# Kernel optimization log

Hardware: AMD Instinct MI355X
Metric: run time of the kernel (lower is better)

Reference implementation:

```python
import jax, jax.numpy as jnp
import numpy as np

N, E, G = 50000, 800000, 64
IN, H, C = 128, 3, 64
HC = H * C


def _conv(x, src, dst, Wq, bq, Wk, bk, Wv, bv, Ws, bs, Wb):
    # node-level projections, then per-edge gather
    q = (x @ Wq + bq).reshape(-1, H, C)[dst]   # [E,H,C]
    k = (x @ Wk + bk).reshape(-1, H, C)[src]
    v = (x @ Wv + bv).reshape(-1, H, C)[src]
    alpha = (q * k).sum(-1) / jnp.sqrt(jnp.float32(C))  # [E,H]
    # segment softmax over incoming edges of each target node
    amax = jax.ops.segment_max(alpha, dst, num_segments=N)
    amax = jnp.where(jnp.isfinite(amax), amax, 0.0)
    ex = jnp.exp(alpha - amax[dst])
    denom = jax.ops.segment_sum(ex, dst, num_segments=N)
    a = ex / (denom[dst] + 1e-16)
    out = jax.ops.segment_sum(a[:, :, None] * v, dst, num_segments=N).reshape(-1, HC)
    # gated skip (beta=True, root_weight=True)
    r = x @ Ws + bs
    beta = jax.nn.sigmoid(jnp.concatenate([out, r, out - r], -1) @ Wb)  # [N,1]
    return beta * r + (1.0 - beta) * out


def setup_inputs() -> dict:
    key = jax.random.key(0)
    ks = jax.random.split(key, 32)
    x = jax.random.normal(ks[0], (N, IN), dtype=jnp.float32)
    edge_index = jax.random.randint(ks[1], (2, E), 0, N, dtype=jnp.int32)
    batch = jnp.sort(jax.random.randint(ks[2], (N,), 0, G, dtype=jnp.int32))
    s = 0.05
    def w(k, shape):
        return jax.random.normal(k, shape, dtype=jnp.float32) * s
    d = {"x": x, "edge_index": edge_index, "batch": batch}
    ins = [IN, HC]
    ki = 3
    for l in range(2):
        din = ins[l]
        d[f"Wq{l}"] = w(ks[ki], (din, HC)); ki += 1
        d[f"bq{l}"] = jnp.zeros((HC,), jnp.float32)
        d[f"Wk{l}"] = w(ks[ki], (din, HC)); ki += 1
        d[f"bk{l}"] = jnp.zeros((HC,), jnp.float32)
        d[f"Wv{l}"] = w(ks[ki], (din, HC)); ki += 1
        d[f"bv{l}"] = jnp.zeros((HC,), jnp.float32)
        d[f"Ws{l}"] = w(ks[ki], (din, HC)); ki += 1
        d[f"bs{l}"] = jnp.zeros((HC,), jnp.float32)
        d[f"Wb{l}"] = w(ks[ki], (3 * HC, 1)); ki += 1
    d["Wlin"] = w(ks[ki], (HC, 1)); ki += 1
    d["blin"] = jnp.zeros((1,), jnp.float32)
    return d


def reference(x, edge_index, batch,
              Wq0, bq0, Wk0, bk0, Wv0, bv0, Ws0, bs0, Wb0,
              Wq1, bq1, Wk1, bk1, Wv1, bv1, Ws1, bs1, Wb1,
              Wlin, blin):
    src, dst = edge_index[0], edge_index[1]
    h = _conv(x, src, dst, Wq0, bq0, Wk0, bk0, Wv0, bv0, Ws0, bs0, Wb0)
    h = jax.nn.elu(h)
    h = _conv(h, src, dst, Wq1, bq1, Wk1, bk1, Wv1, bv1, Ws1, bs1, Wb1)
    h = jax.nn.elu(h)
    # global mean pool over graphs
    cnt = jax.ops.segment_sum(jnp.ones((N,), jnp.float32), batch, num_segments=G)
    pooled = jax.ops.segment_sum(h, batch, num_segments=G) / jnp.maximum(cnt, 1.0)[:, None]
    logits = (pooled @ Wlin + blin).squeeze(-1)  # [G]
    return logits
```

## Files before the change

kernel.cpp:

```cpp
#include <hip/hip_runtime.h>
#include <math.h>

#define NNODES 50000
#define NEDGES 800000
#define NGRAPH 64
#define DIM_IN 128
#define HCDIM  192
#define QKVRW  768

typedef __attribute__((ext_vector_type(8))) short short8;
typedef __attribute__((ext_vector_type(4))) float f32x4;
typedef __attribute__((ext_vector_type(2))) float f32x2;

__device__ __forceinline__ unsigned short f2bf(float f){
  unsigned int u = __float_as_uint(f);
  unsigned int r = (u + 0x7fffu + ((u>>16)&1u)) >> 16;
  return (unsigned short)r;
}

__device__ __forceinline__ float4 bf4_to_f4(uint2 u){
  float4 f;
  f.x = __uint_as_float(u.x<<16);
  f.y = __uint_as_float(u.x & 0xffff0000u);
  f.z = __uint_as_float(u.y<<16);
  f.w = __uint_as_float(u.y & 0xffff0000u);
  return f;
}

__device__ __forceinline__ float4 fp8x4_to_f4(unsigned int u){
  f32x2 lo = __builtin_amdgcn_cvt_pk_f32_fp8((int)u, false);
  f32x2 hi = __builtin_amdgcn_cvt_pk_f32_fp8((int)u, true);
  float4 f; f.x=lo[0]; f.y=lo[1]; f.z=hi[0]; f.w=hi[1];
  return f;
}

__device__ __forceinline__ float wave_sum(float v){
#pragma unroll
  for(int off=32; off>0; off>>=1) v += __shfl_xor(v, off, 64);
  return v;
}

__global__ void zero_i(int* p, int n){
  int i = blockIdx.x*blockDim.x + threadIdx.x;
  if(i<n) p[i]=0;
}

__global__ void zero2_k(int* a, int* b, int n){
  int i = blockIdx.x*blockDim.x + threadIdx.x;
  if(i<n){ a[i]=0; b[i]=0; }
}

__global__ void hist_k(const int* __restrict__ dst, int* __restrict__ counts, int E){
  int e = blockIdx.x*blockDim.x + threadIdx.x;
  if(e<E) atomicAdd(&counts[dst[e]], 1);
}

__global__ void scan_partial(const int* __restrict__ counts, int* __restrict__ bsum, int N){
  __shared__ int lds[256];
  int t = threadIdx.x;
  int idx = blockIdx.x*256 + t;
  int v = (idx<N)? counts[idx] : 0;
  lds[t]=v; __syncthreads();
#pragma unroll
  for(int off=128; off>0; off>>=1){
    if(t<off) lds[t]+=lds[t+off];
    __syncthreads();
  }
  if(t==0) bsum[blockIdx.x]=lds[0];
}

__global__ void scan_bsum(int* bsum, int nb){
  __shared__ int lds[1024];
  int t=threadIdx.x;
  int v=(t<nb)?bsum[t]:0;
  lds[t]=v; __syncthreads();
  int x=v;
#pragma unroll
  for(int off=1; off<1024; off<<=1){
    int y=(t>=off)?lds[t-off]:0;
    __syncthreads();
    x+=y; lds[t]=x;
    __syncthreads();
  }
  if(t<nb) bsum[t]=x-v;
}

__global__ void scan_final(const int* __restrict__ counts, const int* __restrict__ bsum,
                           int* __restrict__ row_ptr, int N){
  __shared__ int lds[256];
  int t=threadIdx.x;
  int idx=blockIdx.x*256+t;
  int v=(idx<N)?counts[idx]:0;
  lds[t]=v; __syncthreads();
  int x=v;
#pragma unroll
  for(int off=1; off<256; off<<=1){
    int y=(t>=off)?lds[t-off]:0;
    __syncthreads();
    x+=y; lds[t]=x;
    __syncthreads();
  }
  if(idx<=N) row_ptr[idx]= bsum[blockIdx.x]+x-v;
}

__global__ void fill_k(const int* __restrict__ src, const int* __restrict__ dst,
                       const int* __restrict__ row_ptr, int* __restrict__ cursor,
                       int* __restrict__ csr_src, int E){
  int e = blockIdx.x*blockDim.x + threadIdx.x;
  if(e<E){
    int d = dst[e];
    int pos = row_ptr[d] + atomicAdd(&cursor[d], 1);
    csr_src[pos] = src[e];
  }
}

__global__ void cast_bf16(const float* __restrict__ X, unsigned short* __restrict__ Xb, int n4){
  int i = blockIdx.x*blockDim.x + threadIdx.x;
  int i4 = i*4;
  if(i4 < n4){
    float4 v = *(const float4*)(X+i4);
    ushort4 o; o.x=f2bf(v.x); o.y=f2bf(v.y); o.z=f2bf(v.z); o.w=f2bf(v.w);
    *(ushort4*)(Xb+i4) = o;
  }
}

__global__ void build_wt(const float* __restrict__ Wq, const float* __restrict__ Wk,
                         const float* __restrict__ Wv, const float* __restrict__ Ws,
                         const float* __restrict__ bq, const float* __restrict__ bk,
                         const float* __restrict__ bv, const float* __restrict__ bs,
                         unsigned short* __restrict__ Wt, float* __restrict__ bcat, int K){
  int idx = blockIdx.x*256 + threadIdx.x;
  if(idx < QKVRW*K){
    int c = idx / K, k = idx % K;
    int mat = c/HCDIM, cm = c%HCDIM;
    const float* W = (mat==0)?Wq:(mat==1)?Wk:(mat==2)?Wv:Ws;
    Wt[(size_t)c*K + k] = f2bf(W[(size_t)k*HCDIM + cm]);
  }
  if(idx < QKVRW){
    int mat = idx/HCDIM, cm = idx%HCDIM;
    const float* b = (mat==0)?bq:(mat==1)?bk:(mat==2)?bv:bs;
    bcat[idx] = b[cm];
  }
}

template<int K>
__global__ __launch_bounds__(256) void gemm_mfma(
    const unsigned short* __restrict__ Xb,
    const unsigned short* __restrict__ Wt,
    const float* __restrict__ bcat,
    unsigned short* __restrict__ QR,
    unsigned char* __restrict__ KV, int N)
{
  constexpr int CPR = K/8;
  __shared__ unsigned short As[128*K];
  __shared__ unsigned short Bs[64*K];
  const int tid = threadIdx.x;
  const int wv = tid>>6;
  const int lane = tid&63;
  const int m0  = blockIdx.x*128;
  const int cb  = blockIdx.y;
  const int mat = cb/3;
  const int nc0 = cb*64;

  constexpr int A_IT = 128*CPR/256;
#pragma unroll
  for(int it=0; it<A_IT; ++it){
    int p = it*256 + tid;
    int r = p/CPR, c = p%CPR;
    int cs = c ^ (r&7);
    int grow = m0 + r; if(grow > N-1) grow = N-1;
    const unsigned short* gp = Xb + (size_t)grow*K + cs*8;
    unsigned short* lp = As + (size_t)(it*256 + wv*64)*8;
    __builtin_amdgcn_global_load_lds(
        (const __attribute__((address_space(1))) unsigned int*)gp,
        (__attribute__((address_space(3))) unsigned int*)lp, 16, 0, 0);
  }
  constexpr int B_IT = 64*CPR/256;
#pragma unroll
  for(int it=0; it<B_IT; ++it){
    int p = it*256 + tid;
    int r = p/CPR, c = p%CPR;
    int cs = c ^ (r&7);
    const unsigned short* gp = Wt + (size_t)(nc0 + r)*K + cs*8;
    unsigned short* lp = Bs + (size_t)(it*256 + wv*64)*8;
    __builtin_amdgcn_global_load_lds(
        (const __attribute__((address_space(1))) unsigned int*)gp,
        (__attribute__((address_space(3))) unsigned int*)lp, 16, 0, 0);
  }
  __syncthreads();

  const int wr = wv>>1, wc = wv&1;
  const int lhi = lane>>4, llo = lane&15;
  f32x4 acc[4][2] = {};
#pragma unroll
  for(int kk=0; kk<K; kk+=32){
    short8 a[4], b[2];
    const int chunk = kk/8 + lhi;
#pragma unroll
    for(int i=0;i<4;++i){
      int rr = wr*64 + i*16 + llo;
      int cs = chunk ^ (rr&7);
      a[i] = *(const short8*)(As + (size_t)rr*K + cs*8);
    }
#pragma unroll
    for(int j=0;j<2;++j){
      int cc = wc*32 + j*16 + llo;
      int cs = chunk ^ (cc&7);
      b[j] = *(const short8*)(Bs + (size_t)cc*K + cs*8);
    }
#pragma unroll
    for(int i=0;i<4;++i)
#pragma unroll
      for(int j=0;j<2;++j)
        acc[i][j] = __builtin_amdgcn_mfma_f32_16x16x32_bf16(a[i], b[j], acc[i][j], 0,0,0);
  }

  const int col0 = nc0 + wc*32 + llo;
  float bias0 = bcat[col0];
  float bias1 = bcat[col0+16];
  if(mat==0 || mat==3){
    const int coff = (mat==0) ? col0 : col0-384;
#pragma unroll
    for(int i=0;i<4;++i){
#pragma unroll
      for(int r=0;r<4;++r){
        int grow = m0 + wr*64 + i*16 + lhi*4 + r;
        if(grow < N){
          size_t base = (size_t)grow*384 + coff;
          QR[base]      = f2bf(acc[i][0][r] + bias0);
          QR[base + 16] = f2bf(acc[i][1][r] + bias1);
        }
      }
    }
  } else {
#pragma unroll
    for(int i=0;i<4;++i){
#pragma unroll
      for(int r=0;r<4;++r){
        int grow = m0 + wr*64 + i*16 + lhi*4 + r;
        float v0 = acc[i][0][r] + bias0;
        float v1 = acc[i][1][r] + bias1;
        float n0 = __shfl_xor(v0, 1, 64);
        float n1 = __shfl_xor(v1, 1, 64);
        if(((llo&1)==0) && grow < N){
          int p0 = __builtin_amdgcn_cvt_pk_fp8_f32(v0, n0, 0, false);
          int p1 = __builtin_amdgcn_cvt_pk_fp8_f32(v1, n1, 0, false);
          unsigned char* kb = KV + (size_t)grow*384 + (col0-192);
          *(unsigned short*)(kb)    = (unsigned short)(p0 & 0xffff);
          *(unsigned short*)(kb+16) = (unsigned short)(p1 & 0xffff);
        }
      }
    }
  }
}

template<bool OUTBF>
__global__ __launch_bounds__(256) void attn_kernel(
  const unsigned short* __restrict__ QR,
  const unsigned char* __restrict__ KV,
  const int* __restrict__ row_ptr, const int* __restrict__ csr_src,
  const float* __restrict__ Wb, float* __restrict__ HoutF,
  unsigned short* __restrict__ HoutB, int N)
{
  const int wave = threadIdx.x>>6;
  const int lane = threadIdx.x&63;
  const int g    = lane>>4;
  const int l    = lane&15;
  const int n = blockIdx.x*4 + wave;
  if(n>=N) return;

  const unsigned short* nr = QR + (size_t)n*384 + 4*l;
  float4 q0 = bf4_to_f4(*(const uint2*)(nr));
  float4 q1 = bf4_to_f4(*(const uint2*)(nr+64));
  float4 q2 = bf4_to_f4(*(const uint2*)(nr+128));

  const int s0 = row_ptr[n];
  const int deg = row_ptr[n+1]-s0;

  float4 a0={0,0,0,0}, a1={0,0,0,0}, a2={0,0,0,0};
  float d0=0.f,d1=0.f,d2=0.f;

  int sCur = csr_src[s0 + (g<deg ? g : 0)];
  for(int base=0; base<deg; base+=4){
    const int inext = base + 4 + g;
    const int sNxt = csr_src[s0 + (inext<deg ? inext : 0)];
    const bool valid = (base + g < deg);
    const unsigned int* kv = (const unsigned int*)(KV + (size_t)sCur*384) + l;
    unsigned int ku0 = kv[0],  ku1 = kv[16], ku2 = kv[32];
    unsigned int vu0 = kv[48], vu1 = kv[64], vu2 = kv[80];
    float4 k0 = fp8x4_to_f4(ku0);
    float4 k1 = fp8x4_to_f4(ku1);
    float4 k2 = fp8x4_to_f4(ku2);
    float p0 = q0.x*k0.x+q0.y*k0.y+q0.z*k0.z+q0.w*k0.w;
    float p1 = q1.x*k1.x+q1.y*k1.y+q1.z*k1.z+q1.w*k1.w;
    float p2 = q2.x*k2.x+q2.y*k2.y+q2.z*k2.z+q2.w*k2.w;
#pragma unroll
    for(int off=1; off<16; off<<=1){
      p0 += __shfl_xor(p0, off, 64);
      p1 += __shfl_xor(p1, off, 64);
      p2 += __shfl_xor(p2, off, 64);
    }
    float e0 = valid ? __expf(0.125f*p0) : 0.f;
    float e1 = valid ? __expf(0.125f*p1) : 0.f;
    float e2 = valid ? __expf(0.125f*p2) : 0.f;
    d0 += e0; d1 += e1; d2 += e2;
    float4 v0 = fp8x4_to_f4(vu0);
    float4 v1 = fp8x4_to_f4(vu1);
    float4 v2 = fp8x4_to_f4(vu2);
    a0.x+=e0*v0.x; a0.y+=e0*v0.y; a0.z+=e0*v0.z; a0.w+=e0*v0.w;
    a1.x+=e1*v1.x; a1.y+=e1*v1.y; a1.z+=e1*v1.z; a1.w+=e1*v1.w;
    a2.x+=e2*v2.x; a2.y+=e2*v2.y; a2.z+=e2*v2.z; a2.w+=e2*v2.w;
    sCur = sNxt;
  }

#pragma unroll
  for(int off=16; off<64; off<<=1){
    a0.x+=__shfl_xor(a0.x,off,64); a0.y+=__shfl_xor(a0.y,off,64);
    a0.z+=__shfl_xor(a0.z,off,64); a0.w+=__shfl_xor(a0.w,off,64);
    a1.x+=__shfl_xor(a1.x,off,64); a1.y+=__shfl_xor(a1.y,off,64);
    a1.z+=__shfl_xor(a1.z,off,64); a1.w+=__shfl_xor(a1.w,off,64);
    a2.x+=__shfl_xor(a2.x,off,64); a2.y+=__shfl_xor(a2.y,off,64);
    a2.z+=__shfl_xor(a2.z,off,64); a2.w+=__shfl_xor(a2.w,off,64);
    d0+=__shfl_xor(d0,off,64); d1+=__shfl_xor(d1,off,64); d2+=__shfl_xor(d2,off,64);
  }
  const float id0=1.f/(d0+1e-16f), id1=1.f/(d1+1e-16f), id2=1.f/(d2+1e-16f);
  float4 o0, o1, o2;
  o0.x=a0.x*id0; o0.y=a0.y*id0; o0.z=a0.z*id0; o0.w=a0.w*id0;
  o1.x=a1.x*id1; o1.y=a1.y*id1; o1.z=a1.z*id1; o1.w=a1.w*id1;
  o2.x=a2.x*id2; o2.y=a2.y*id2; o2.z=a2.z*id2; o2.w=a2.w*id2;

  float4 r0 = bf4_to_f4(*(const uint2*)(nr+192));
  float4 r1 = bf4_to_f4(*(const uint2*)(nr+256));
  float4 r2 = bf4_to_f4(*(const uint2*)(nr+320));

  const float* wb = Wb + 4*l;
  float4 w00=*(const float4*)(wb),     w01=*(const float4*)(wb+64),  w02=*(const float4*)(wb+128);
  float4 w10=*(const float4*)(wb+192), w11=*(const float4*)(wb+256), w12=*(const float4*)(wb+320);
  float4 w20=*(const float4*)(wb+384), w21=*(const float4*)(wb+448), w22=*(const float4*)(wb+512);
  float z =
    o0.x*w00.x+o0.y*w00.y+o0.z*w00.z+o0.w*w00.w +
    o1.x*w01.x+o1.y*w01.y+o1.z*w01.z+o1.w*w01.w +
    o2.x*w02.x+o2.y*w02.y+o2.z*w02.z+o2.w*w02.w +
    r0.x*w10.x+r0.y*w10.y+r0.z*w10.z+r0.w*w10.w +
    r1.x*w11.x+r1.y*w11.y+r1.z*w11.z+r1.w*w11.w +
    r2.x*w12.x+r2.y*w12.y+r2.z*w12.z+r2.w*w12.w +
    (o0.x-r0.x)*w20.x+(o0.y-r0.y)*w20.y+(o0.z-r0.z)*w20.z+(o0.w-r0.w)*w20.w +
    (o1.x-r1.x)*w21.x+(o1.y-r1.y)*w21.y+(o1.z-r1.z)*w21.z+(o1.w-r1.w)*w21.w +
    (o2.x-r2.x)*w22.x+(o2.y-r2.y)*w22.y+(o2.z-r2.z)*w22.z+(o2.w-r2.w)*w22.w;
#pragma unroll
  for(int off=1; off<16; off<<=1) z += __shfl_xor(z, off, 64);
  const float beta = 1.f/(1.f+__expf(-z));
  float4 h0,h1,h2;
  h0.x=beta*r0.x+(1.f-beta)*o0.x; h0.y=beta*r0.y+(1.f-beta)*o0.y;
  h0.z=beta*r0.z+(1.f-beta)*o0.z; h0.w=beta*r0.w+(1.f-beta)*o0.w;
  h1.x=beta*r1.x+(1.f-beta)*o1.x; h1.y=beta*r1.y+(1.f-beta)*o1.y;
  h1.z=beta*r1.z+(1.f-beta)*o1.z; h1.w=beta*r1.w+(1.f-beta)*o1.w;
  h2.x=beta*r2.x+(1.f-beta)*o2.x; h2.y=beta*r2.y+(1.f-beta)*o2.y;
  h2.z=beta*r2.z+(1.f-beta)*o2.z; h2.w=beta*r2.w+(1.f-beta)*o2.w;
  h0.x=(h0.x>0.f)?h0.x:expm1f(h0.x); h0.y=(h0.y>0.f)?h0.y:expm1f(h0.y);
  h0.z=(h0.z>0.f)?h0.z:expm1f(h0.z); h0.w=(h0.w>0.f)?h0.w:expm1f(h0.w);
  h1.x=(h1.x>0.f)?h1.x:expm1f(h1.x); h1.y=(h1.y>0.f)?h1.y:expm1f(h1.y);
  h1.z=(h1.z>0.f)?h1.z:expm1f(h1.z); h1.w=(h1.w>0.f)?h1.w:expm1f(h1.w);
  h2.x=(h2.x>0.f)?h2.x:expm1f(h2.x); h2.y=(h2.y>0.f)?h2.y:expm1f(h2.y);
  h2.z=(h2.z>0.f)?h2.z:expm1f(h2.z); h2.w=(h2.w>0.f)?h2.w:expm1f(h2.w);
  if(g==0){
    if(OUTBF){
      unsigned short* hb = HoutB + (size_t)n*HCDIM + 4*l;
      ushort4 u0, u1, u2;
      u0.x=f2bf(h0.x); u0.y=f2bf(h0.y); u0.z=f2bf(h0.z); u0.w=f2bf(h0.w);
      u1.x=f2bf(h1.x); u1.y=f2bf(h1.y); u1.z=f2bf(h1.z); u1.w=f2bf(h1.w);
      u2.x=f2bf(h2.x); u2.y=f2bf(h2.y); u2.z=f2bf(h2.z); u2.w=f2bf(h2.w);
      *(ushort4*)(hb)     = u0;
      *(ushort4*)(hb+64)  = u1;
      *(ushort4*)(hb+128) = u2;
    } else {
      float* ho = HoutF + (size_t)n*HCDIM + 4*l;
      *(float4*)(ho)     = h0;
      *(float4*)(ho+64)  = h1;
      *(float4*)(ho+128) = h2;
    }
  }
}

__global__ void zero_pool(float* pooled, int* cnt){
  int i = blockIdx.x*256 + threadIdx.x;
  if(i < NGRAPH*HCDIM) ((int*)pooled)[i]=0;
  if(i < NGRAPH) cnt[i]=0;
}

__global__ void cnt_k(const int* __restrict__ batch, int* __restrict__ cnt, int N){
  __shared__ int h[NGRAPH];
  const int t = threadIdx.x;
  if(t<NGRAPH) h[t]=0;
  __syncthreads();
  int i = blockIdx.x*blockDim.x + t;
  if(i<N) atomicAdd(&h[batch[i]], 1);
  __syncthreads();
  if(t<NGRAPH && h[t]) atomicAdd(&cnt[t], h[t]);
}

__global__ void pool_k(const float* __restrict__ H, const int* __restrict__ batch,
                       float* __restrict__ pooled, int N){
  const int t = threadIdx.x;
  int start = blockIdx.x*256;
  int end = min(start+256, N);
  if(start>=N) return;
  int cur = batch[start];
  float acc = 0.f;
  for(int nn=start; nn<end; ++nn){
    int g = batch[nn];
    if(g!=cur){ atomicAdd(&pooled[(size_t)cur*HCDIM+t], acc); acc=0.f; cur=g; }
    acc += H[(size_t)nn*HCDIM+t];
  }
  atomicAdd(&pooled[(size_t)cur*HCDIM+t], acc);
}

__global__ void logits_k(const float* __restrict__ pooled, const int* __restrict__ cnt,
                         const float* __restrict__ Wlin, const float* __restrict__ blin,
                         float* __restrict__ out){
  const int g = blockIdx.x;
  const int lane = threadIdx.x;
  float c = fmaxf((float)cnt[g], 1.f);
  float s = 0.f;
#pragma unroll
  for(int j=0;j<3;++j){
    int col = j*64+lane;
    s += pooled[(size_t)g*HCDIM+col]/c * Wlin[col];
  }
  s = wave_sum(s);
  if(lane==0) out[g] = s + blin[0];
}

extern "C" void kernel_launch(void* const* d_in, const int* in_sizes, int n_in,
                              void* d_out, int out_size, void* d_ws, size_t ws_size,
                              hipStream_t stream)
{
  const int N=NNODES, E=NEDGES;
  const float* x     = (const float*)d_in[0];
  const int*   ei    = (const int*)d_in[1];
  const int*   batch = (const int*)d_in[2];
  const int* esrc = ei;
  const int* edst = ei + E;
  const float* Wq0=(const float*)d_in[3];  const float* bq0=(const float*)d_in[4];
  const float* Wk0=(const float*)d_in[5];  const float* bk0=(const float*)d_in[6];
  const float* Wv0=(const float*)d_in[7];  const float* bv0=(const float*)d_in[8];
  const float* Ws0=(const float*)d_in[9];  const float* bs0=(const float*)d_in[10];
  const float* Wb0=(const float*)d_in[11];
  const float* Wq1=(const float*)d_in[12]; const float* bq1=(const float*)d_in[13];
  const float* Wk1=(const float*)d_in[14]; const float* bk1=(const float*)d_in[15];
  const float* Wv1=(const float*)d_in[16]; const float* bv1=(const float*)d_in[17];
  const float* Ws1=(const float*)d_in[18]; const float* bs1=(const float*)d_in[19];
  const float* Wb1=(const float*)d_in[20];
  const float* Wlin=(const float*)d_in[21];
  const float* blin=(const float*)d_in[22];
  float* out = (float*)d_out;

  char* p = (char*)d_ws;
  auto alloc = [&](size_t bytes)->char*{
    char* q = p; p += (bytes+255)/256*256; return q;
  };
  unsigned short* Xb   = (unsigned short*)alloc((size_t)N*HCDIM*2);
  unsigned short* QR   = (unsigned short*)alloc((size_t)N*384*2);
  unsigned char*  KV   = (unsigned char*)alloc((size_t)N*384);
  float* H1            = (float*)alloc((size_t)N*HCDIM*4);
  unsigned short* Wt   = (unsigned short*)alloc((size_t)QKVRW*HCDIM*2);
  float* bcat          = (float*)alloc(QKVRW*4);
  int* counts  = (int*)alloc((size_t)N*4);
  int* cursor  = (int*)alloc((size_t)N*4);
  int* row_ptr = (int*)alloc((size_t)(N+1)*4);
  int* csr     = (int*)alloc((size_t)E*4);
  int* bsum    = (int*)alloc(4096);
  float* pooled= (float*)alloc((size_t)NGRAPH*HCDIM*4);
  int* cnt     = (int*)alloc(256);

  const int NB = (N+255)/256;

  zero2_k<<<(N+255)/256,256,0,stream>>>(counts,cursor,N);
  hist_k<<<(E+255)/256,256,0,stream>>>(edst,counts,E);
  scan_partial<<<NB,256,0,stream>>>(counts,bsum,N);
  scan_bsum<<<1,1024,0,stream>>>(bsum,NB);
  scan_final<<<NB,256,0,stream>>>(counts,bsum,row_ptr,N);
  fill_k<<<(E+255)/256,256,0,stream>>>(esrc,edst,row_ptr,cursor,csr,E);

  dim3 ggemm((N+127)/128, 12);
  cast_bf16<<<((N*DIM_IN/4)+255)/256,256,0,stream>>>(x, Xb, N*DIM_IN);
  build_wt<<<(QKVRW*DIM_IN+255)/256,256,0,stream>>>(Wq0,Wk0,Wv0,Ws0,bq0,bk0,bv0,bs0,Wt,bcat,DIM_IN);
  gemm_mfma<DIM_IN><<<ggemm,256,0,stream>>>(Xb,Wt,bcat,QR,KV,N);
  attn_kernel<true><<<(N+3)/4,256,0,stream>>>(QR,KV,row_ptr,csr,Wb0,nullptr,Xb,N);
  build_wt<<<(QKVRW*HCDIM+255)/256,256,0,stream>>>(Wq1,Wk1,Wv1,Ws1,bq1,bk1,bv1,bs1,Wt,bcat,HCDIM);
  gemm_mfma<HCDIM><<<ggemm,256,0,stream>>>(Xb,Wt,bcat,QR,KV,N);
  attn_kernel<false><<<(N+3)/4,256,0,stream>>>(QR,KV,row_ptr,csr,Wb1,H1,nullptr,N);

  zero_pool<<<(NGRAPH*HCDIM+255)/256,256,0,stream>>>(pooled,cnt);
  cnt_k<<<(N+255)/256,256,0,stream>>>(batch,cnt,N);
  pool_k<<<(N+255)/256,192,0,stream>>>(H1,batch,pooled,N);
  logits_k<<<NGRAPH,64,0,stream>>>(pooled,cnt,Wlin,blin,out);
}
```

Before: 432.8 us.

## Process eight edges per wave in attention and K-tile the projection GEMM

```diff
diff --git a/kernel.cpp b/kernel.cpp
--- a/kernel.cpp
+++ b/kernel.cpp
@@ -151,9 +151,8 @@
     unsigned short* __restrict__ QR,
     unsigned char* __restrict__ KV, int N)
 {
-  constexpr int CPR = K/8;
-  __shared__ unsigned short As[128*K];
-  __shared__ unsigned short Bs[64*K];
+  __shared__ unsigned short As[128*64];
+  __shared__ unsigned short Bs[64*64];
   const int tid = threadIdx.x;
   const int wv = tid>>6;
   const int lane = tid&63;
@@ -162,57 +161,61 @@
   const int mat = cb/3;
   const int nc0 = cb*64;
 
-  constexpr int A_IT = 128*CPR/256;
-#pragma unroll
-  for(int it=0; it<A_IT; ++it){
-    int p = it*256 + tid;
-    int r = p/CPR, c = p%CPR;
-    int cs = c ^ (r&7);
-    int grow = m0 + r; if(grow > N-1) grow = N-1;
-    const unsigned short* gp = Xb + (size_t)grow*K + cs*8;
-    unsigned short* lp = As + (size_t)(it*256 + wv*64)*8;
-    __builtin_amdgcn_global_load_lds(
-        (const __attribute__((address_space(1))) unsigned int*)gp,
-        (__attribute__((address_space(3))) unsigned int*)lp, 16, 0, 0);
-  }
-  constexpr int B_IT = 64*CPR/256;
-#pragma unroll
-  for(int it=0; it<B_IT; ++it){
-    int p = it*256 + tid;
-    int r = p/CPR, c = p%CPR;
-    int cs = c ^ (r&7);
-    const unsigned short* gp = Wt + (size_t)(nc0 + r)*K + cs*8;
-    unsigned short* lp = Bs + (size_t)(it*256 + wv*64)*8;
-    __builtin_amdgcn_global_load_lds(
-        (const __attribute__((address_space(1))) unsigned int*)gp,
-        (__attribute__((address_space(3))) unsigned int*)lp, 16, 0, 0);
-  }
-  __syncthreads();
-
   const int wr = wv>>1, wc = wv&1;
   const int lhi = lane>>4, llo = lane&15;
   f32x4 acc[4][2] = {};
-#pragma unroll
-  for(int kk=0; kk<K; kk+=32){
-    short8 a[4], b[2];
-    const int chunk = kk/8 + lhi;
-#pragma unroll
-    for(int i=0;i<4;++i){
-      int rr = wr*64 + i*16 + llo;
-      int cs = chunk ^ (rr&7);
-      a[i] = *(const short8*)(As + (size_t)rr*K + cs*8);
-    }
-#pragma unroll
-    for(int j=0;j<2;++j){
-      int cc = wc*32 + j*16 + llo;
-      int cs = chunk ^ (cc&7);
-      b[j] = *(const short8*)(Bs + (size_t)cc*K + cs*8);
-    }
-#pragma unroll
-    for(int i=0;i<4;++i)
-#pragma unroll
-      for(int j=0;j<2;++j)
-        acc[i][j] = __builtin_amdgcn_mfma_f32_16x16x32_bf16(a[i], b[j], acc[i][j], 0,0,0);
+
+  constexpr int NT = K/64;
+#pragma unroll
+  for(int kt=0; kt<NT; ++kt){
+    if(kt>0) __syncthreads();
+#pragma unroll
+    for(int it=0; it<4; ++it){
+      int p = it*256 + tid;
+      int r = p>>3, c = p&7;
+      int cs = c ^ (r&7);
+      int grow = m0 + r; if(grow > N-1) grow = N-1;
+      const unsigned short* gp = Xb + (size_t)grow*K + kt*64 + cs*8;
+      unsigned short* lp = As + (size_t)(it*256 + wv*64)*8;
+      __builtin_amdgcn_global_load_lds(
+          (const __attribute__((address_space(1))) unsigned int*)gp,
+          (__attribute__((address_space(3))) unsigned int*)lp, 16, 0, 0);
+    }
+#pragma unroll
+    for(int it=0; it<2; ++it){
+      int p = it*256 + tid;
+      int r = p>>3, c = p&7;
+      int cs = c ^ (r&7);
+      const unsigned short* gp = Wt + (size_t)(nc0 + r)*K + kt*64 + cs*8;
+      unsigned short* lp = Bs + (size_t)(it*256 + wv*64)*8;
+      __builtin_amdgcn_global_load_lds(
+          (const __attribute__((address_space(1))) unsigned int*)gp,
+          (__attribute__((address_space(3))) unsigned int*)lp, 16, 0, 0);
+    }
+    __syncthreads();
+
+#pragma unroll
+    for(int kk=0; kk<64; kk+=32){
+      short8 a[4], b[2];
+      const int chunk = (kk>>3) + lhi;
+#pragma unroll
+      for(int i=0;i<4;++i){
+        int rr = wr*64 + i*16 + llo;
+        int cs = chunk ^ (rr&7);
+        a[i] = *(const short8*)(As + rr*64 + cs*8);
+      }
+#pragma unroll
+      for(int j=0;j<2;++j){
+        int cc = wc*32 + j*16 + llo;
+        int cs = chunk ^ (cc&7);
+        b[j] = *(const short8*)(Bs + cc*64 + cs*8);
+      }
+#pragma unroll
+      for(int i=0;i<4;++i)
+#pragma unroll
+        for(int j=0;j<2;++j)
+          acc[i][j] = __builtin_amdgcn_mfma_f32_16x16x32_bf16(a[i], b[j], acc[i][j], 0,0,0);
+    }
   }
 
   const int col0 = nc0 + wc*32 + llo;
@@ -264,120 +267,132 @@
 {
   const int wave = threadIdx.x>>6;
   const int lane = threadIdx.x&63;
-  const int g    = lane>>4;
-  const int l    = lane&15;
+  const int g    = lane>>3;
+  const int j    = lane&7;
   const int n = blockIdx.x*4 + wave;
   if(n>=N) return;
 
-  const unsigned short* nr = QR + (size_t)n*384 + 4*l;
-  float4 q0 = bf4_to_f4(*(const uint2*)(nr));
-  float4 q1 = bf4_to_f4(*(const uint2*)(nr+64));
-  float4 q2 = bf4_to_f4(*(const uint2*)(nr+128));
+  float4 qL[3], qH[3];
+#pragma unroll
+  for(int h=0;h<3;++h){
+    uint4 uu = *(const uint4*)(QR + (size_t)n*384 + h*64 + j*8);
+    qL[h] = bf4_to_f4(make_uint2(uu.x,uu.y));
+    qH[h] = bf4_to_f4(make_uint2(uu.z,uu.w));
+  }
 
   const int s0 = row_ptr[n];
   const int deg = row_ptr[n+1]-s0;
 
-  float4 a0={0,0,0,0}, a1={0,0,0,0}, a2={0,0,0,0};
-  float d0=0.f,d1=0.f,d2=0.f;
+  float4 aL[3]={{0,0,0,0},{0,0,0,0},{0,0,0,0}};
+  float4 aH[3]={{0,0,0,0},{0,0,0,0},{0,0,0,0}};
+  float dsum[3]={0,0,0};
 
   int sCur = csr_src[s0 + (g<deg ? g : 0)];
-  for(int base=0; base<deg; base+=4){
-    const int inext = base + 4 + g;
+  for(int base=0; base<deg; base+=8){
+    const int inext = base + 8 + g;
     const int sNxt = csr_src[s0 + (inext<deg ? inext : 0)];
     const bool valid = (base + g < deg);
-    const unsigned int* kv = (const unsigned int*)(KV + (size_t)sCur*384) + l;
-    unsigned int ku0 = kv[0],  ku1 = kv[16], ku2 = kv[32];
-    unsigned int vu0 = kv[48], vu1 = kv[64], vu2 = kv[80];
-    float4 k0 = fp8x4_to_f4(ku0);
-    float4 k1 = fp8x4_to_f4(ku1);
-    float4 k2 = fp8x4_to_f4(ku2);
-    float p0 = q0.x*k0.x+q0.y*k0.y+q0.z*k0.z+q0.w*k0.w;
-    float p1 = q1.x*k1.x+q1.y*k1.y+q1.z*k1.z+q1.w*k1.w;
-    float p2 = q2.x*k2.x+q2.y*k2.y+q2.z*k2.z+q2.w*k2.w;
-#pragma unroll
-    for(int off=1; off<16; off<<=1){
-      p0 += __shfl_xor(p0, off, 64);
-      p1 += __shfl_xor(p1, off, 64);
-      p2 += __shfl_xor(p2, off, 64);
-    }
-    float e0 = valid ? __expf(0.125f*p0) : 0.f;
-    float e1 = valid ? __expf(0.125f*p1) : 0.f;
-    float e2 = valid ? __expf(0.125f*p2) : 0.f;
-    d0 += e0; d1 += e1; d2 += e2;
-    float4 v0 = fp8x4_to_f4(vu0);
-    float4 v1 = fp8x4_to_f4(vu1);
-    float4 v2 = fp8x4_to_f4(vu2);
-    a0.x+=e0*v0.x; a0.y+=e0*v0.y; a0.z+=e0*v0.z; a0.w+=e0*v0.w;
-    a1.x+=e1*v1.x; a1.y+=e1*v1.y; a1.z+=e1*v1.z; a1.w+=e1*v1.w;
-    a2.x+=e2*v2.x; a2.y+=e2*v2.y; a2.z+=e2*v2.z; a2.w+=e2*v2.w;
+    const unsigned int* kv = (const unsigned int*)(KV + (size_t)sCur*384);
+    float p[3];
+#pragma unroll
+    for(int h=0;h<3;++h){
+      unsigned int k0 = kv[h*16 + j*2];
+      unsigned int k1 = kv[h*16 + j*2 + 1];
+      float4 kA = fp8x4_to_f4(k0);
+      float4 kB = fp8x4_to_f4(k1);
+      p[h] = qL[h].x*kA.x + qL[h].y*kA.y + qL[h].z*kA.z + qL[h].w*kA.w
+           + qH[h].x*kB.x + qH[h].y*kB.y + qH[h].z*kB.z + qH[h].w*kB.w;
+    }
+#pragma unroll
+    for(int off=1; off<8; off<<=1){
+      p[0] += __shfl_xor(p[0], off, 64);
+      p[1] += __shfl_xor(p[1], off, 64);
+      p[2] += __shfl_xor(p[2], off, 64);
+    }
+    float e0 = valid ? __expf(0.125f*p[0]) : 0.f;
+    float e1 = valid ? __expf(0.125f*p[1]) : 0.f;
+    float e2 = valid ? __expf(0.125f*p[2]) : 0.f;
+    dsum[0]+=e0; dsum[1]+=e1; dsum[2]+=e2;
+    float ee[3] = {e0,e1,e2};
+#pragma unroll
+    for(int h=0;h<3;++h){
+      unsigned int v0 = kv[48 + h*16 + j*2];
+      unsigned int v1 = kv[48 + h*16 + j*2 + 1];
+      float4 vA = fp8x4_to_f4(v0);
+      float4 vB = fp8x4_to_f4(v1);
+      aL[h].x+=ee[h]*vA.x; aL[h].y+=ee[h]*vA.y; aL[h].z+=ee[h]*vA.z; aL[h].w+=ee[h]*vA.w;
+      aH[h].x+=ee[h]*vB.x; aH[h].y+=ee[h]*vB.y; aH[h].z+=ee[h]*vB.z; aH[h].w+=ee[h]*vB.w;
+    }
     sCur = sNxt;
   }
 
 #pragma unroll
-  for(int off=16; off<64; off<<=1){
-    a0.x+=__shfl_xor(a0.x,off,64); a0.y+=__shfl_xor(a0.y,off,64);
-    a0.z+=__shfl_xor(a0.z,off,64); a0.w+=__shfl_xor(a0.w,off,64);
-    a1.x+=__shfl_xor(a1.x,off,64); a1.y+=__shfl_xor(a1.y,off,64);
-    a1.z+=__shfl_xor(a1.z,off,64); a1.w+=__shfl_xor(a1.w,off,64);
-    a2.x+=__shfl_xor(a2.x,off,64); a2.y+=__shfl_xor(a2.y,off,64);
-    a2.z+=__shfl_xor(a2.z,off,64); a2.w+=__shfl_xor(a2.w,off,64);
-    d0+=__shfl_xor(d0,off,64); d1+=__shfl_xor(d1,off,64); d2+=__shfl_xor(d2,off,64);
-  }
-  const float id0=1.f/(d0+1e-16f), id1=1.f/(d1+1e-16f), id2=1.f/(d2+1e-16f);
-  float4 o0, o1, o2;
-  o0.x=a0.x*id0; o0.y=a0.y*id0; o0.z=a0.z*id0; o0.w=a0.w*id0;
-  o1.x=a1.x*id1; o1.y=a1.y*id1; o1.z=a1.z*id1; o1.w=a1.w*id1;
-  o2.x=a2.x*id2; o2.y=a2.y*id2; o2.z=a2.z*id2; o2.w=a2.w*id2;
-
-  float4 r0 = bf4_to_f4(*(const uint2*)(nr+192));
-  float4 r1 = bf4_to_f4(*(const uint2*)(nr+256));
-  float4 r2 = bf4_to_f4(*(const uint2*)(nr+320));
-
-  const float* wb = Wb + 4*l;
-  float4 w00=*(const float4*)(wb),     w01=*(const float4*)(wb+64),  w02=*(const float4*)(wb+128);
-  float4 w10=*(const float4*)(wb+192), w11=*(const float4*)(wb+256), w12=*(const float4*)(wb+320);
-  float4 w20=*(const float4*)(wb+384), w21=*(const float4*)(wb+448), w22=*(const float4*)(wb+512);
-  float z =
-    o0.x*w00.x+o0.y*w00.y+o0.z*w00.z+o0.w*w00.w +
-    o1.x*w01.x+o1.y*w01.y+o1.z*w01.z+o1.w*w01.w +
-    o2.x*w02.x+o2.y*w02.y+o2.z*w02.z+o2.w*w02.w +
-    r0.x*w10.x+r0.y*w10.y+r0.z*w10.z+r0.w*w10.w +
-    r1.x*w11.x+r1.y*w11.y+r1.z*w11.z+r1.w*w11.w +
-    r2.x*w12.x+r2.y*w12.y+r2.z*w12.z+r2.w*w12.w +
-    (o0.x-r0.x)*w20.x+(o0.y-r0.y)*w20.y+(o0.z-r0.z)*w20.z+(o0.w-r0.w)*w20.w +
-    (o1.x-r1.x)*w21.x+(o1.y-r1.y)*w21.y+(o1.z-r1.z)*w21.z+(o1.w-r1.w)*w21.w +
-    (o2.x-r2.x)*w22.x+(o2.y-r2.y)*w22.y+(o2.z-r2.z)*w22.z+(o2.w-r2.w)*w22.w;
-#pragma unroll
-  for(int off=1; off<16; off<<=1) z += __shfl_xor(z, off, 64);
+  for(int off=8; off<64; off<<=1){
+#pragma unroll
+    for(int h=0;h<3;++h){
+      aL[h].x+=__shfl_xor(aL[h].x,off,64); aL[h].y+=__shfl_xor(aL[h].y,off,64);
+      aL[h].z+=__shfl_xor(aL[h].z,off,64); aL[h].w+=__shfl_xor(aL[h].w,off,64);
+      aH[h].x+=__shfl_xor(aH[h].x,off,64); aH[h].y+=__shfl_xor(aH[h].y,off,64);
+      aH[h].z+=__shfl_xor(aH[h].z,off,64); aH[h].w+=__shfl_xor(aH[h].w,off,64);
+      dsum[h]+=__shfl_xor(dsum[h],off,64);
+    }
+  }
+
+  float4 oL[3], oH[3], rL[3], rH[3];
+#pragma unroll
+  for(int h=0;h<3;++h){
+    float id = 1.f/(dsum[h]+1e-16f);
+    oL[h].x=aL[h].x*id; oL[h].y=aL[h].y*id; oL[h].z=aL[h].z*id; oL[h].w=aL[h].w*id;
+    oH[h].x=aH[h].x*id; oH[h].y=aH[h].y*id; oH[h].z=aH[h].z*id; oH[h].w=aH[h].w*id;
+    uint4 uu = *(const uint4*)(QR + (size_t)n*384 + 192 + h*64 + j*8);
+    rL[h] = bf4_to_f4(make_uint2(uu.x,uu.y));
+    rH[h] = bf4_to_f4(make_uint2(uu.z,uu.w));
+  }
+
+  float z = 0.f;
+#pragma unroll
+  for(int h=0;h<3;++h){
+    const int c = h*64 + j*8;
+    float4 woL=*(const float4*)(Wb+c),     woH=*(const float4*)(Wb+c+4);
+    float4 wrL=*(const float4*)(Wb+192+c), wrH=*(const float4*)(Wb+192+c+4);
+    float4 wdL=*(const float4*)(Wb+384+c), wdH=*(const float4*)(Wb+384+c+4);
+    z += oL[h].x*woL.x+oL[h].y*woL.y+oL[h].z*woL.z+oL[h].w*woL.w
+       + oH[h].x*woH.x+oH[h].y*woH.y+oH[h].z*woH.z+oH[h].w*woH.w
+       + rL[h].x*wrL.x+rL[h].y*wrL.y+rL[h].z*wrL.z+rL[h].w*wrL.w
+       + rH[h].x*wrH.x+rH[h].y*wrH.y+rH[h].z*wrH.z+rH[h].w*wrH.w
+       + (oL[h].x-rL[h].x)*wdL.x+(oL[h].y-rL[h].y)*wdL.y
+       + (oL[h].z-rL[h].z)*wdL.z+(oL[h].w-rL[h].w)*wdL.w
+       + (oH[h].x-rH[h].x)*wdH.x+(oH[h].y-rH[h].y)*wdH.y
+       + (oH[h].z-rH[h].z)*wdH.z+(oH[h].w-rH[h].w)*wdH.w;
+  }
+#pragma unroll
+  for(int off=1; off<8; off<<=1) z += __shfl_xor(z, off, 64);
   const float beta = 1.f/(1.f+__expf(-z));
-  float4 h0,h1,h2;
-  h0.x=beta*r0.x+(1.f-beta)*o0.x; h0.y=beta*r0.y+(1.f-beta)*o0.y;
-  h0.z=beta*r0.z+(1.f-beta)*o0.z; h0.w=beta*r0.w+(1.f-beta)*o0.w;
-  h1.x=beta*r1.x+(1.f-beta)*o1.x; h1.y=beta*r1.y+(1.f-beta)*o1.y;
-  h1.z=beta*r1.z+(1.f-beta)*o1.z; h1.w=beta*r1.w+(1.f-beta)*o1.w;
-  h2.x=beta*r2.x+(1.f-beta)*o2.x; h2.y=beta*r2.y+(1.f-beta)*o2.y;
-  h2.z=beta*r2.z+(1.f-beta)*o2.z; h2.w=beta*r2.w+(1.f-beta)*o2.w;
-  h0.x=(h0.x>0.f)?h0.x:expm1f(h0.x); h0.y=(h0.y>0.f)?h0.y:expm1f(h0.y);
-  h0.z=(h0.z>0.f)?h0.z:expm1f(h0.z); h0.w=(h0.w>0.f)?h0.w:expm1f(h0.w);
-  h1.x=(h1.x>0.f)?h1.x:expm1f(h1.x); h1.y=(h1.y>0.f)?h1.y:expm1f(h1.y);
-  h1.z=(h1.z>0.f)?h1.z:expm1f(h1.z); h1.w=(h1.w>0.f)?h1.w:expm1f(h1.w);
-  h2.x=(h2.x>0.f)?h2.x:expm1f(h2.x); h2.y=(h2.y>0.f)?h2.y:expm1f(h2.y);
-  h2.z=(h2.z>0.f)?h2.z:expm1f(h2.z); h2.w=(h2.w>0.f)?h2.w:expm1f(h2.w);
+
   if(g==0){
-    if(OUTBF){
-      unsigned short* hb = HoutB + (size_t)n*HCDIM + 4*l;
-      ushort4 u0, u1, u2;
-      u0.x=f2bf(h0.x); u0.y=f2bf(h0.y); u0.z=f2bf(h0.z); u0.w=f2bf(h0.w);
-      u1.x=f2bf(h1.x); u1.y=f2bf(h1.y); u1.z=f2bf(h1.z); u1.w=f2bf(h1.w);
-      u2.x=f2bf(h2.x); u2.y=f2bf(h2.y); u2.z=f2bf(h2.z); u2.w=f2bf(h2.w);
-      *(ushort4*)(hb)     = u0;
-      *(ushort4*)(hb+64)  = u1;
-      *(ushort4*)(hb+128) = u2;
-    } else {
-      float* ho = HoutF + (size_t)n*HCDIM + 4*l;
-      *(float4*)(ho)     = h0;
-      *(float4*)(ho+64)  = h1;
-      *(float4*)(ho+128) = h2;
+#pragma unroll
+    for(int h=0;h<3;++h){
+      float4 hL, hH;
+      hL.x=beta*rL[h].x+(1.f-beta)*oL[h].x; hL.y=beta*rL[h].y+(1.f-beta)*oL[h].y;
+      hL.z=beta*rL[h].z+(1.f-beta)*oL[h].z; hL.w=beta*rL[h].w+(1.f-beta)*oL[h].w;
+      hH.x=beta*rH[h].x+(1.f-beta)*oH[h].x; hH.y=beta*rH[h].y+(1.f-beta)*oH[h].y;
+      hH.z=beta*rH[h].z+(1.f-beta)*oH[h].z; hH.w=beta*rH[h].w+(1.f-beta)*oH[h].w;
+      hL.x=(hL.x>0.f)?hL.x:expm1f(hL.x); hL.y=(hL.y>0.f)?hL.y:expm1f(hL.y);
+      hL.z=(hL.z>0.f)?hL.z:expm1f(hL.z); hL.w=(hL.w>0.f)?hL.w:expm1f(hL.w);
+      hH.x=(hH.x>0.f)?hH.x:expm1f(hH.x); hH.y=(hH.y>0.f)?hH.y:expm1f(hH.y);
+      hH.z=(hH.z>0.f)?hH.z:expm1f(hH.z); hH.w=(hH.w>0.f)?hH.w:expm1f(hH.w);
+      if(OUTBF){
+        unsigned short* hb = HoutB + (size_t)n*HCDIM + h*64 + j*8;
+        ushort4 uL, uH;
+        uL.x=f2bf(hL.x); uL.y=f2bf(hL.y); uL.z=f2bf(hL.z); uL.w=f2bf(hL.w);
+        uH.x=f2bf(hH.x); uH.y=f2bf(hH.y); uH.z=f2bf(hH.z); uH.w=f2bf(hH.w);
+        *(ushort4*)(hb)   = uL;
+        *(ushort4*)(hb+4) = uH;
+      } else {
+        float* ho = HoutF + (size_t)n*HCDIM + h*64 + j*8;
+        *(float4*)(ho)   = hL;
+        *(float4*)(ho+4) = hH;
+      }
     }
   }
 }
```

Measured after the change: 483.4 us. +11.7%, slower.
